# Kernel optimization log

Hardware: AMD Instinct MI355X
Metric: run time of the kernel (lower is better)

Reference implementation:

```python
import math
import jax, jax.numpy as jnp
import numpy as np

B, N, D = 32, 1025, 768
K, CD, TD = 64, 128, 256  # num_clusters, cluster_dim, token_dim
REG = 0.1
NUM_ITERS = 5


def setup_inputs() -> dict:
    key = jax.random.key(0)
    ks = jax.random.split(key, 8)
    x = jax.random.normal(ks[0], (B, N, D), dtype=jnp.float32)
    # Linear params (torch nn.Linear: y = x @ W.T + b; we store W already transposed as [in, out])
    Wf = jax.random.normal(ks[1], (D, CD), dtype=jnp.float32) / math.sqrt(D)
    bf = jnp.zeros((CD,), dtype=jnp.float32)
    Ws = jax.random.normal(ks[2], (D, K), dtype=jnp.float32) / math.sqrt(D)
    bs = jnp.zeros((K,), dtype=jnp.float32)
    Wt = jax.random.normal(ks[3], (D, TD), dtype=jnp.float32) / math.sqrt(D)
    bt = jnp.zeros((TD,), dtype=jnp.float32)
    anchors = jax.random.normal(ks[4], (K, CD), dtype=jnp.float32) * 0.1
    dust_bin = jnp.float32(1.0)
    sharpness = jnp.float32(5.0)
    return {"x": x, "Wf": Wf, "bf": bf, "Ws": Ws, "bs": bs, "Wt": Wt, "bt": bt,
            "anchors": anchors, "dust_bin": dust_bin, "sharpness": sharpness}


def _log_otp_solver(log_a, log_b, M, num_iters, reg):
    M = M / reg
    u = jnp.zeros_like(log_a)  # [B, K+1]
    v = jnp.zeros_like(log_b)  # [B, N-1]
    for _ in range(num_iters):
        u = log_a - jax.nn.logsumexp(M + v[:, None, :], axis=2)
        v = log_b - jax.nn.logsumexp(M + u[:, :, None], axis=1)
    return M + u[:, :, None] + v[:, None, :]


def reference(x, Wf, bf, Ws, bs, Wt, bt, anchors, dust_bin, sharpness):
    b, n, d = x.shape
    t_global = x[:, 0]            # [B, D]
    fi = x[:, 1:]                 # [B, N-1, D]
    f = fi @ Wf + bf              # [B, N-1, CD]
    s = jnp.swapaxes(fi @ Ws + bs, 1, 2)  # [B, K, N-1]
    t = t_global @ Wt + bt        # [B, TD]
    s = s * sharpness
    dust = jnp.broadcast_to(dust_bin, (b, 1, n - 1))
    s_aug = jnp.concatenate([s, dust], axis=1)  # [B, K+1, N-1]
    log_a = jnp.full((b, K + 1), -math.log(K + 1), dtype=x.dtype)
    log_b = jnp.full((b, n - 1), -math.log(n - 1), dtype=x.dtype)
    log_P = _log_otp_solver(log_a, log_b, s_aug, NUM_ITERS, REG)
    p = jnp.exp(log_P)[:, :-1, :]  # [B, K, N-1]
    # v_agg = sum_n p[b,k,n] * (2*f[b,n,:] - anchors[k,:])  (algebraic rewrite of the broadcast sum)
    v_agg = 2.0 * jnp.einsum('bkn,bnc->bkc', p, f) - p.sum(axis=2)[:, :, None] * anchors[None]
    v_local = v_agg.reshape(b, -1)            # [B, K*CD]
    f_out = jnp.concatenate([t, v_local], axis=-1)
    norm = jnp.maximum(jnp.linalg.norm(f_out, axis=-1, keepdims=True), 1e-12)
    return f_out / norm
```

## Files before the change

### kernel.cpp

```cpp
#include <hip/hip_runtime.h>
#include <math.h>


#define BATCH 32
#define NTOK  1025
#define DIM   768
#define KDIM  64
#define CDIM  128
#define TDIM  256
#define NM1   1024
#define ROWLEN 8448
#define NITER 5
#define INV_REG 10.0f
#define NSPLIT 16
#define LOG_A (-4.17438727f)
#define LOG_B (-6.93147181f)

typedef __attribute__((ext_vector_type(8))) short short8;
typedef __attribute__((ext_vector_type(4))) float floatx4;

typedef __attribute__((address_space(3))) unsigned int lds_uint;
typedef const __attribute__((address_space(1))) unsigned int glb_uint;

__device__ __forceinline__ void gload_lds16(const void* g, void* l) {
    __builtin_amdgcn_global_load_lds((glb_uint*)g, (lds_uint*)l, 16, 0, 0);
}

__device__ __forceinline__ unsigned short bf16_rne(float f) {
    unsigned u = __builtin_bit_cast(unsigned, f);
    unsigned r = u + 0x7FFFu + ((u >> 16) & 1u);
    return (unsigned short)(r >> 16);
}

__device__ __forceinline__ short8 cvt8(float4 a, float4 b) {
    short8 r;
    r[0] = (short)bf16_rne(a.x); r[1] = (short)bf16_rne(a.y);
    r[2] = (short)bf16_rne(a.z); r[3] = (short)bf16_rne(a.w);
    r[4] = (short)bf16_rne(b.x); r[5] = (short)bf16_rne(b.y);
    r[6] = (short)bf16_rne(b.z); r[7] = (short)bf16_rne(b.w);
    return r;
}

__global__ __launch_bounds__(256) void pack_w(
    const float* __restrict__ Wf, const float* __restrict__ Ws,
    const float* __restrict__ bf, const float* __restrict__ bs,
    short* __restrict__ W_pack, float* __restrict__ bias_all)
{
    int idx = blockIdx.x * 256 + threadIdx.x;
    if (idx < 24 * 12 * 512) {
        int g    = idx / 6144;
        int rem  = idx - g * 6144;
        int nf   = rem >> 9;
        int rem2 = rem & 511;
        int lane = rem2 >> 3;
        int j    = rem2 & 7;
        int k = g * 32 + (lane >> 4) * 8 + j;
        int c = nf * 16 + (lane & 15);
        float v = (c < CDIM) ? Wf[(size_t)k * CDIM + c] : Ws[(size_t)k * KDIM + (c - CDIM)];
        W_pack[idx] = (short)bf16_rne(v);
    }
    if (idx < 192) bias_all[idx] = (idx < CDIM) ? bf[idx] : bs[idx - CDIM];
}

__global__ __launch_bounds__(256, 2) void gemm_fs(
    const float* __restrict__ x, const short* __restrict__ W_pack,
    const float* __restrict__ bias_all, const float* __restrict__ sharp_p,
    float* __restrict__ fmat, float* __restrict__ Mmat)
{
    __shared__ __align__(16) short Bs[12288];
    __shared__ __align__(16) short As[4096];
    const int tid  = threadIdx.x;
    const int wave = tid >> 6, lane = tid & 63;
    const int quad = lane >> 4, lrow = lane & 15;
    const int R = blockIdx.x * 64 + wave * 16;

    const int arow = blockIdx.x * 64 + (tid >> 2);
    const float* asrc = x + ((size_t)(arow >> 10) * NTOK + 1 + (arow & 1023)) * DIM + (tid & 3) * 16;
    const int r    = (tid >> 2) & 15;
    const int seg  = tid & 3;
    const int kk_w = seg >> 1;
    const int q0   = (seg & 1) * 2;
    short* adst0 = &As[(((tid >> 6) * 2 + kk_w) * 64 + q0 * 16 + r) * 8];
    short* adst1 = &As[(((tid >> 6) * 2 + kk_w) * 64 + (q0 + 1) * 16 + r) * 8];

    floatx4 acc[12];
#pragma unroll
    for (int nf = 0; nf < 12; ++nf) acc[nf] = (floatx4){0.f, 0.f, 0.f, 0.f};

    for (int ko = 0; ko < 12; ++ko) {
        __syncthreads();
        const short* bsrc = W_pack + ko * 12288 + tid * 8;
#pragma unroll
        for (int i = 0; i < 6; ++i)
            gload_lds16(bsrc + i * 2048, &Bs[i * 2048 + tid * 8]);
        {
            const float* ap = asrc + ko * 64;
            float4 g0 = *(const float4*)(ap);
            float4 g1 = *(const float4*)(ap + 4);
            float4 g2 = *(const float4*)(ap + 8);
            float4 g3 = *(const float4*)(ap + 12);
            *(short8*)adst0 = cvt8(g0, g1);
            *(short8*)adst1 = cvt8(g2, g3);
        }
        __syncthreads();
#pragma unroll
        for (int kk = 0; kk < 2; ++kk) {
            short8 af = *(const short8*)&As[((wave * 2 + kk) * 64 + lane) * 8];
#pragma unroll
            for (int nf = 0; nf < 12; ++nf) {
                short8 bf8 = *(const short8*)&Bs[((kk * 12 + nf) * 64 + lane) * 8];
                acc[nf] = __builtin_amdgcn_mfma_f32_16x16x32_bf16(af, bf8, acc[nf], 0, 0, 0);
            }
        }
    }

    const float sc = sharp_p[0] * INV_REG;
    const int bb = R >> 10;
    const int n0 = (R & 1023) + quad * 4;
#pragma unroll
    for (int nf = 0; nf < 12; ++nf) {
        const int c = nf * 16 + lrow;
        const float bias = bias_all[c];
        if (nf < 8) {
            float* fp = fmat + ((size_t)R + quad * 4) * CDIM + c;
#pragma unroll
            for (int j = 0; j < 4; ++j)
                fp[(size_t)j * CDIM] = acc[nf][j] + bias;
        } else {
            const int k = c - CDIM;
            float4 w = make_float4((acc[nf][0] + bias) * sc, (acc[nf][1] + bias) * sc,
                                   (acc[nf][2] + bias) * sc, (acc[nf][3] + bias) * sc);
            *(float4*)(Mmat + ((size_t)bb * KDIM + k) * NM1 + n0) = w;
        }
    }
}

__global__ __launch_bounds__(256) void gemm_t_split(
    const float* __restrict__ x, const float* __restrict__ Wt,
    float* __restrict__ tpart)
{
    __shared__ float xr[256];
    const int b = blockIdx.x, dy = blockIdx.y, c = threadIdx.x;
    xr[c] = x[(size_t)b * NTOK * DIM + (size_t)dy * 256 + c];
    __syncthreads();
    float acc = 0.f;
    const float* wp = Wt + (size_t)dy * 256 * TDIM + c;
#pragma unroll 8
    for (int d = 0; d < 256; ++d) acc = fmaf(xr[d], wp[(size_t)d * TDIM], acc);
    tpart[((size_t)dy * BATCH + b) * TDIM + c] = acc;
}

__global__ __launch_bounds__(256) void sink_u(
    const float* __restrict__ Mmat, const float* __restrict__ v_in,
    const float* __restrict__ dust_p, float* __restrict__ u_out)
{
    const int wv   = (blockIdx.x << 2) + (threadIdx.x >> 6);
    const int lane = threadIdx.x & 63;
    const int b = wv / 65, k = wv - b * 65;
    const float dustM = dust_p[0] * INV_REG;

    const float4* vp = (const float4*)(v_in + (size_t)b * NM1);
    float xs[16];
    if (k < 64) {
        const float4* Mp = (const float4*)(Mmat + ((size_t)b * KDIM + k) * NM1);
#pragma unroll
        for (int i = 0; i < 4; ++i) {
            float4 mv = Mp[i * 64 + lane];
            float4 vv = vp[i * 64 + lane];
            xs[i * 4 + 0] = mv.x + vv.x;
            xs[i * 4 + 1] = mv.y + vv.y;
            xs[i * 4 + 2] = mv.z + vv.z;
            xs[i * 4 + 3] = mv.w + vv.w;
        }
    } else {
#pragma unroll
        for (int i = 0; i < 4; ++i) {
            float4 vv = vp[i * 64 + lane];
            xs[i * 4 + 0] = dustM + vv.x;
            xs[i * 4 + 1] = dustM + vv.y;
            xs[i * 4 + 2] = dustM + vv.z;
            xs[i * 4 + 3] = dustM + vv.w;
        }
    }
    float m = xs[0];
#pragma unroll
    for (int i = 1; i < 16; ++i) m = fmaxf(m, xs[i]);
#pragma unroll
    for (int off = 1; off < 64; off <<= 1) m = fmaxf(m, __shfl_xor(m, off));
    float S = 0.f;
#pragma unroll
    for (int i = 0; i < 16; ++i) S += __expf(xs[i] - m);
#pragma unroll
    for (int off = 1; off < 64; off <<= 1) S += __shfl_xor(S, off);
    if (lane == 0) u_out[wv] = LOG_A - (m + __logf(S));
}

__global__ __launch_bounds__(256) void sink_v(
    const float* __restrict__ Mmat, const float* __restrict__ u_in,
    const float* __restrict__ dust_p, float* __restrict__ v_out)
{
    __shared__ float us[65];
    const int b = blockIdx.x, tid = threadIdx.x;
    const int n = blockIdx.y * 256 + tid;
    if (tid < 65) us[tid] = u_in[b * 65 + tid];
    __syncthreads();
    const float* Mb = Mmat + (size_t)b * KDIM * NM1 + n;
    float xs[64];
#pragma unroll
    for (int k = 0; k < 64; ++k) xs[k] = Mb[(size_t)k * NM1] + us[k];
    const float xd = dust_p[0] * INV_REG + us[64];
    float m = xd;
#pragma unroll
    for (int k = 0; k < 64; ++k) m = fmaxf(m, xs[k]);
    float S = __expf(xd - m);
#pragma unroll
    for (int k = 0; k < 64; ++k) S += __expf(xs[k] - m);
    v_out[(size_t)b * NM1 + n] = LOG_B - (m + __logf(S));
}

__global__ __launch_bounds__(128) void aggregate(
    const float* __restrict__ Mmat, const float* __restrict__ fmat,
    const float* __restrict__ u_in, const float* __restrict__ v_in,
    float* __restrict__ vpart, float* __restrict__ rspart)
{
    __shared__ float fs[32 * 128];
    __shared__ float ps[32 * 68];
    __shared__ float us[KDIM];
    __shared__ float vsh[64];
    const int b = blockIdx.x, ns = blockIdx.y;
    const int tid = threadIdx.x;
    const int tx = tid & 7;
    const int ty = tid >> 3;
    const int n0 = ns * 64;

    if (tid < 64) us[tid] = u_in[b * 65 + tid];
    else          vsh[tid - 64] = v_in[(size_t)b * NM1 + n0 + (tid - 64)];

    const float* Mb = Mmat + (size_t)b * KDIM * NM1;
    const float* fb = fmat + ((size_t)b * NM1 + n0) * CDIM;

    float acc[8][8];
#pragma unroll
    for (int i = 0; i < 8; ++i)
#pragma unroll
        for (int j = 0; j < 8; ++j) acc[i][j] = 0.f;
    float rsacc = 0.f;

    const int p_nn = tid & 31;
    const int p_kb = tid >> 5;

    for (int ch = 0; ch < 2; ++ch) {
        __syncthreads();
        {
            const float* fsrc = fb + (size_t)(ch * 32) * CDIM;
#pragma unroll
            for (int q = 0; q < 8; ++q) {
                int idx = q * 128 + tid;
                int nn = idx >> 5, c4 = (idx & 31) * 4;
                *(float4*)&fs[nn * 128 + c4] = *(const float4*)(fsrc + (size_t)nn * CDIM + c4);
            }
        }
        {
            int nglob = n0 + ch * 32 + p_nn;
            float vv = vsh[ch * 32 + p_nn];
#pragma unroll
            for (int q = 0; q < 16; ++q) {
                int k = q * 4 + p_kb;
                ps[p_nn * 68 + k] = __expf(Mb[(size_t)k * NM1 + nglob] + us[k] + vv);
            }
        }
        __syncthreads();
        if (tid < 64) {
#pragma unroll
            for (int nn = 0; nn < 32; ++nn) rsacc += ps[nn * 68 + tid];
        }
#pragma unroll
        for (int nn = 0; nn < 32; ++nn) {
            float4 p0 = *(const float4*)&ps[nn * 68 + tx * 8];
            float4 p1 = *(const float4*)&ps[nn * 68 + tx * 8 + 4];
            float4 f0 = *(const float4*)&fs[nn * 128 + ty * 8];
            float4 f1 = *(const float4*)&fs[nn * 128 + ty * 8 + 4];
            float pv[8] = {p0.x, p0.y, p0.z, p0.w, p1.x, p1.y, p1.z, p1.w};
            float fv[8] = {f0.x, f0.y, f0.z, f0.w, f1.x, f1.y, f1.z, f1.w};
#pragma unroll
            for (int i = 0; i < 8; ++i)
#pragma unroll
                for (int j = 0; j < 8; ++j)
                    acc[i][j] = fmaf(pv[i], fv[j], acc[i][j]);
        }
    }

    float* vp = vpart + (size_t)(ns * BATCH + b) * (KDIM * CDIM);
#pragma unroll
    for (int i = 0; i < 8; ++i) {
        int k = tx * 8 + i;
        float4 w0 = make_float4(acc[i][0], acc[i][1], acc[i][2], acc[i][3]);
        float4 w1 = make_float4(acc[i][4], acc[i][5], acc[i][6], acc[i][7]);
        float* wp = vp + (size_t)k * CDIM + ty * 8;
        *(float4*)(wp)     = w0;
        *(float4*)(wp + 4) = w1;
    }
    if (tid < 64) rspart[(ns * BATCH + b) * KDIM + tid] = rsacc;
}

__global__ __launch_bounds__(256) void reduce_vagg(
    const float* __restrict__ vpart, const float* __restrict__ rspart,
    const float* __restrict__ anchors, float* __restrict__ vagg,
    float* __restrict__ sq)
{
    __shared__ float rst[8];
    __shared__ float red[4];
    const int b = blockIdx.x, segi = blockIdx.y, tid = threadIdx.x;
    const int lane = tid & 63, wave = tid >> 6;
    if (tid < 8) {
        float s = 0.f;
#pragma unroll
        for (int ns = 0; ns < NSPLIT; ++ns)
            s += rspart[(ns * BATCH + b) * KDIM + segi * 8 + tid];
        rst[tid] = s;
    }
    __syncthreads();
    const int i4 = segi * 256 + tid;
    float4 s = make_float4(0.f, 0.f, 0.f, 0.f);
#pragma unroll
    for (int ns = 0; ns < NSPLIT; ++ns) {
        const float4 v = *(const float4*)&vpart[(size_t)(ns * BATCH + b) * (KDIM * CDIM) + (size_t)i4 * 4];
        s.x += v.x; s.y += v.y; s.z += v.z; s.w += v.w;
    }
    float rs = rst[tid >> 5];
    const float4 an = *(const float4*)&anchors[(size_t)i4 * 4];
    float4 v;
    v.x = 2.f * s.x - rs * an.x;
    v.y = 2.f * s.y - rs * an.y;
    v.z = 2.f * s.z - rs * an.z;
    v.w = 2.f * s.w - rs * an.w;
    *(float4*)&vagg[(size_t)b * (KDIM * CDIM) + (size_t)i4 * 4] = v;
    float ss = v.x * v.x + v.y * v.y + v.z * v.z + v.w * v.w;
#pragma unroll
    for (int off = 32; off > 0; off >>= 1) ss += __shfl_down(ss, off);
    if (lane == 0) red[wave] = ss;
    __syncthreads();
    if (tid == 0) sq[b * 8 + segi] = red[0] + red[1] + red[2] + red[3];
}

__global__ __launch_bounds__(256) void finalize2(
    const float* __restrict__ tpart, const float* __restrict__ bt,
    const float* __restrict__ sq, const float* __restrict__ vagg,
    float* __restrict__ out)
{
    __shared__ float red[4];
    __shared__ float sc_sh;
    const int b = blockIdx.x, tid = threadIdx.x;
    const int lane = tid & 63, wave = tid >> 6;

    float t = bt[tid];
#pragma unroll
    for (int s = 0; s < 3; ++s) t += tpart[((size_t)s * BATCH + b) * TDIM + tid];
    float ss = t * t;
#pragma unroll
    for (int off = 32; off > 0; off >>= 1) ss += __shfl_down(ss, off);
    if (lane == 0) red[wave] = ss;
    __syncthreads();
    if (tid == 0) {
        float tot = red[0] + red[1] + red[2] + red[3];
#pragma unroll
        for (int i = 0; i < 8; ++i) tot += sq[b * 8 + i];
        sc_sh = 1.f / fmaxf(sqrtf(tot), 1e-12f);
    }
    __syncthreads();
    const float scale = sc_sh;
    float* orow = out + (size_t)b * ROWLEN;
    orow[tid] = t * scale;
    const float* va = vagg + (size_t)b * (KDIM * CDIM);
#pragma unroll
    for (int q = 0; q < 8; ++q) {
        int i4 = q * 256 + tid;
        float4 v = *(const float4*)&va[(size_t)i4 * 4];
        v.x *= scale; v.y *= scale; v.z *= scale; v.w *= scale;
        *(float4*)&orow[TDIM + (size_t)i4 * 4] = v;
    }
}

extern "C" void kernel_launch(void* const* d_in, const int* in_sizes, int n_in,
                              void* d_out, int out_size, void* d_ws, size_t ws_size,
                              hipStream_t stream)
{
    const float* x       = (const float*)d_in[0];
    const float* Wf      = (const float*)d_in[1];
    const float* bf      = (const float*)d_in[2];
    const float* Ws      = (const float*)d_in[3];
    const float* bs      = (const float*)d_in[4];
    const float* Wt      = (const float*)d_in[5];
    const float* bt      = (const float*)d_in[6];
    const float* anchors = (const float*)d_in[7];
    const float* dust    = (const float*)d_in[8];
    const float* sharp   = (const float*)d_in[9];
    float* out = (float*)d_out;

    char* base = (char*)d_ws;
    short* W_pack   = (short*)base;
    float* bias_all = (float*)(base + 294912);
    float* Mmat     = bias_all + 192;
    float* fmat     = Mmat + (size_t)BATCH * KDIM * NM1;
    float* u_buf    = fmat + (size_t)BATCH * NM1 * CDIM;
    float* v_buf    = u_buf + BATCH * 65;
    float* vpart    = v_buf + BATCH * NM1;
    float* rspart   = vpart + (size_t)NSPLIT * BATCH * KDIM * CDIM;
    float* tpart    = rspart + NSPLIT * BATCH * KDIM;
    float* sq       = tpart + 3 * BATCH * TDIM;
    float* vagg     = Mmat;

    hipLaunchKernelGGL(pack_w, dim3(576), dim3(256), 0, stream,
                       Wf, Ws, bf, bs, W_pack, bias_all);
    hipLaunchKernelGGL(gemm_fs, dim3(512), dim3(256), 0, stream,
                       x, W_pack, bias_all, sharp, fmat, Mmat);
    hipLaunchKernelGGL(gemm_t_split, dim3(BATCH, 3), dim3(256), 0, stream,
                       x, Wt, tpart);

    hipMemsetAsync(v_buf, 0, (size_t)BATCH * NM1 * sizeof(float), stream);
    for (int it = 0; it < NITER; ++it) {
        hipLaunchKernelGGL(sink_u, dim3(520), dim3(256), 0, stream,
                           Mmat, v_buf, dust, u_buf);
        hipLaunchKernelGGL(sink_v, dim3(BATCH, 4), dim3(256), 0, stream,
                           Mmat, u_buf, dust, v_buf);
    }

    hipLaunchKernelGGL(aggregate, dim3(BATCH, NSPLIT), dim3(128), 0, stream,
                       Mmat, fmat, u_buf, v_buf, vpart, rspart);
    hipLaunchKernelGGL(reduce_vagg, dim3(BATCH, 8), dim3(256), 0, stream,
                       vpart, rspart, anchors, vagg, sq);
    hipLaunchKernelGGL(finalize2, dim3(BATCH), dim3(256), 0, stream,
                       tpart, bt, sq, vagg, out);
}
```

Before: 257.9 us.

## Prefetch GEMM A tiles, specialize first Sinkhorn step, and widen sink_v/aggregate grids

Software-prefetches the next A tile in gemm_fs into registers so global loads overlap the MFMA loop. The first sink_u is specialized to skip reading v, which removes the memset. sink_v runs twice as many 128-thread blocks. aggregate moves to NSPLIT=32 with 256 threads, each handling 32 tokens in one pass, giving more parallelism at the cost of twice the partial sums for reduce_vagg to read.

```diff
diff --git a/kernel.cpp b/kernel.cpp
--- a/kernel.cpp
+++ b/kernel.cpp
@@ -12,7 +12,7 @@
 #define ROWLEN 8448
 #define NITER 5
 #define INV_REG 10.0f
-#define NSPLIT 16
+#define NSPLIT 32
 #define LOG_A (-4.17438727f)
 #define LOG_B (-6.93147181f)
 
@@ -87,20 +87,25 @@
 #pragma unroll
     for (int nf = 0; nf < 12; ++nf) acc[nf] = (floatx4){0.f, 0.f, 0.f, 0.f};
 
+    float4 g0 = *(const float4*)(asrc);
+    float4 g1 = *(const float4*)(asrc + 4);
+    float4 g2 = *(const float4*)(asrc + 8);
+    float4 g3 = *(const float4*)(asrc + 12);
+
     for (int ko = 0; ko < 12; ++ko) {
         __syncthreads();
         const short* bsrc = W_pack + ko * 12288 + tid * 8;
 #pragma unroll
         for (int i = 0; i < 6; ++i)
             gload_lds16(bsrc + i * 2048, &Bs[i * 2048 + tid * 8]);
-        {
-            const float* ap = asrc + ko * 64;
-            float4 g0 = *(const float4*)(ap);
-            float4 g1 = *(const float4*)(ap + 4);
-            float4 g2 = *(const float4*)(ap + 8);
-            float4 g3 = *(const float4*)(ap + 12);
-            *(short8*)adst0 = cvt8(g0, g1);
-            *(short8*)adst1 = cvt8(g2, g3);
+        *(short8*)adst0 = cvt8(g0, g1);
+        *(short8*)adst1 = cvt8(g2, g3);
+        if (ko < 11) {
+            const float* ap = asrc + (ko + 1) * 64;
+            g0 = *(const float4*)(ap);
+            g1 = *(const float4*)(ap + 4);
+            g2 = *(const float4*)(ap + 8);
+            g3 = *(const float4*)(ap + 12);
         }
         __syncthreads();
 #pragma unroll
@@ -150,6 +155,7 @@
     tpart[((size_t)dy * BATCH + b) * TDIM + c] = acc;
 }
 
+template<bool FIRST>
 __global__ __launch_bounds__(256) void sink_u(
     const float* __restrict__ Mmat, const float* __restrict__ v_in,
     const float* __restrict__ dust_p, float* __restrict__ u_out)
@@ -166,7 +172,7 @@
 #pragma unroll
         for (int i = 0; i < 4; ++i) {
             float4 mv = Mp[i * 64 + lane];
-            float4 vv = vp[i * 64 + lane];
+            float4 vv = FIRST ? make_float4(0.f, 0.f, 0.f, 0.f) : vp[i * 64 + lane];
             xs[i * 4 + 0] = mv.x + vv.x;
             xs[i * 4 + 1] = mv.y + vv.y;
             xs[i * 4 + 2] = mv.z + vv.z;
@@ -175,7 +181,7 @@
     } else {
 #pragma unroll
         for (int i = 0; i < 4; ++i) {
-            float4 vv = vp[i * 64 + lane];
+            float4 vv = FIRST ? make_float4(0.f, 0.f, 0.f, 0.f) : vp[i * 64 + lane];
             xs[i * 4 + 0] = dustM + vv.x;
             xs[i * 4 + 1] = dustM + vv.y;
             xs[i * 4 + 2] = dustM + vv.z;
@@ -195,13 +201,13 @@
     if (lane == 0) u_out[wv] = LOG_A - (m + __logf(S));
 }
 
-__global__ __launch_bounds__(256) void sink_v(
+__global__ __launch_bounds__(128) void sink_v(
     const float* __restrict__ Mmat, const float* __restrict__ u_in,
     const float* __restrict__ dust_p, float* __restrict__ v_out)
 {
     __shared__ float us[65];
     const int b = blockIdx.x, tid = threadIdx.x;
-    const int n = blockIdx.y * 256 + tid;
+    const int n = blockIdx.y * 128 + tid;
     if (tid < 65) us[tid] = u_in[b * 65 + tid];
     __syncthreads();
     const float* Mb = Mmat + (size_t)b * KDIM * NM1 + n;
@@ -218,7 +224,7 @@
     v_out[(size_t)b * NM1 + n] = LOG_B - (m + __logf(S));
 }
 
-__global__ __launch_bounds__(128) void aggregate(
+__global__ __launch_bounds__(256) void aggregate(
     const float* __restrict__ Mmat, const float* __restrict__ fmat,
     const float* __restrict__ u_in, const float* __restrict__ v_in,
     float* __restrict__ vpart, float* __restrict__ rspart)
@@ -226,79 +232,66 @@
     __shared__ float fs[32 * 128];
     __shared__ float ps[32 * 68];
     __shared__ float us[KDIM];
-    __shared__ float vsh[64];
+    __shared__ float vsh[32];
     const int b = blockIdx.x, ns = blockIdx.y;
     const int tid = threadIdx.x;
     const int tx = tid & 7;
     const int ty = tid >> 3;
-    const int n0 = ns * 64;
+    const int n0 = ns * 32;
 
     if (tid < 64) us[tid] = u_in[b * 65 + tid];
-    else          vsh[tid - 64] = v_in[(size_t)b * NM1 + n0 + (tid - 64)];
-
-    const float* Mb = Mmat + (size_t)b * KDIM * NM1;
+    else if (tid < 96) vsh[tid - 64] = v_in[(size_t)b * NM1 + n0 + (tid - 64)];
+    __syncthreads();
+
     const float* fb = fmat + ((size_t)b * NM1 + n0) * CDIM;
-
-    float acc[8][8];
+#pragma unroll
+    for (int q = 0; q < 4; ++q) {
+        int idx = q * 256 + tid;
+        int nn = idx >> 5, c4 = (idx & 31) * 4;
+        *(float4*)&fs[nn * 128 + c4] = *(const float4*)(fb + (size_t)nn * CDIM + c4);
+    }
+    {
+        const int p_nn = tid & 31, p_kb = tid >> 5;
+        const float* Mb = Mmat + (size_t)b * KDIM * NM1 + n0 + p_nn;
+        const float vv = vsh[p_nn];
+#pragma unroll
+        for (int q = 0; q < 8; ++q) {
+            int k = q * 8 + p_kb;
+            ps[p_nn * 68 + k] = __expf(Mb[(size_t)k * NM1] + us[k] + vv);
+        }
+    }
+    __syncthreads();
+
+    float rsacc = 0.f;
+    if (tid < 64) {
+#pragma unroll
+        for (int nn = 0; nn < 32; ++nn) rsacc += ps[nn * 68 + tid];
+    }
+    float acc[8][4];
 #pragma unroll
     for (int i = 0; i < 8; ++i)
 #pragma unroll
-        for (int j = 0; j < 8; ++j) acc[i][j] = 0.f;
-    float rsacc = 0.f;
-
-    const int p_nn = tid & 31;
-    const int p_kb = tid >> 5;
-
-    for (int ch = 0; ch < 2; ++ch) {
-        __syncthreads();
-        {
-            const float* fsrc = fb + (size_t)(ch * 32) * CDIM;
-#pragma unroll
-            for (int q = 0; q < 8; ++q) {
-                int idx = q * 128 + tid;
-                int nn = idx >> 5, c4 = (idx & 31) * 4;
-                *(float4*)&fs[nn * 128 + c4] = *(const float4*)(fsrc + (size_t)nn * CDIM + c4);
-            }
-        }
-        {
-            int nglob = n0 + ch * 32 + p_nn;
-            float vv = vsh[ch * 32 + p_nn];
-#pragma unroll
-            for (int q = 0; q < 16; ++q) {
-                int k = q * 4 + p_kb;
-                ps[p_nn * 68 + k] = __expf(Mb[(size_t)k * NM1 + nglob] + us[k] + vv);
-            }
-        }
-        __syncthreads();
-        if (tid < 64) {
-#pragma unroll
-            for (int nn = 0; nn < 32; ++nn) rsacc += ps[nn * 68 + tid];
-        }
-#pragma unroll
-        for (int nn = 0; nn < 32; ++nn) {
-            float4 p0 = *(const float4*)&ps[nn * 68 + tx * 8];
-            float4 p1 = *(const float4*)&ps[nn * 68 + tx * 8 + 4];
-            float4 f0 = *(const float4*)&fs[nn * 128 + ty * 8];
-            float4 f1 = *(const float4*)&fs[nn * 128 + ty * 8 + 4];
-            float pv[8] = {p0.x, p0.y, p0.z, p0.w, p1.x, p1.y, p1.z, p1.w};
-            float fv[8] = {f0.x, f0.y, f0.z, f0.w, f1.x, f1.y, f1.z, f1.w};
-#pragma unroll
-            for (int i = 0; i < 8; ++i)
-#pragma unroll
-                for (int j = 0; j < 8; ++j)
-                    acc[i][j] = fmaf(pv[i], fv[j], acc[i][j]);
-        }
+        for (int j = 0; j < 4; ++j) acc[i][j] = 0.f;
+#pragma unroll
+    for (int nn = 0; nn < 32; ++nn) {
+        float4 p0 = *(const float4*)&ps[nn * 68 + tx * 8];
+        float4 p1 = *(const float4*)&ps[nn * 68 + tx * 8 + 4];
+        float4 f0 = *(const float4*)&fs[nn * 128 + ty * 4];
+        float pv[8] = {p0.x, p0.y, p0.z, p0.w, p1.x, p1.y, p1.z, p1.w};
+        float fv[4] = {f0.x, f0.y, f0.z, f0.w};
+#pragma unroll
+        for (int i = 0; i < 8; ++i)
+#pragma unroll
+            for (int j = 0; j < 4; ++j)
+                acc[i][j] = fmaf(pv[i], fv[j], acc[i][j]);
     }
 
     float* vp = vpart + (size_t)(ns * BATCH + b) * (KDIM * CDIM);
 #pragma unroll
     for (int i = 0; i < 8; ++i) {
         int k = tx * 8 + i;
-        float4 w0 = make_float4(acc[i][0], acc[i][1], acc[i][2], acc[i][3]);
-        float4 w1 = make_float4(acc[i][4], acc[i][5], acc[i][6], acc[i][7]);
-        float* wp = vp + (size_t)k * CDIM + ty * 8;
-        *(float4*)(wp)     = w0;
-        *(float4*)(wp + 4) = w1;
+        *(float4*)(vp + (size_t)k * CDIM + ty * 4) =
+            make_float4(acc[i][0], acc[i][1], acc[i][2], acc[i][3]);
     }
     if (tid < 64) rspart[(ns * BATCH + b) * KDIM + tid] = rsacc;
 }
@@ -417,15 +410,18 @@
     hipLaunchKernelGGL(gemm_t_split, dim3(BATCH, 3), dim3(256), 0, stream,
                        x, Wt, tpart);
 
-    hipMemsetAsync(v_buf, 0, (size_t)BATCH * NM1 * sizeof(float), stream);
-    for (int it = 0; it < NITER; ++it) {
-        hipLaunchKernelGGL(sink_u, dim3(520), dim3(256), 0, stream,
+    hipLaunchKernelGGL(HIP_KERNEL_NAME(sink_u<true>), dim3(520), dim3(256), 0, stream,
+                       Mmat, v_buf, dust, u_buf);
+    hipLaunchKernelGGL(sink_v, dim3(BATCH, 8), dim3(128), 0, stream,
+                       Mmat, u_buf, dust, v_buf);
+    for (int it = 1; it < NITER; ++it) {
+        hipLaunchKernelGGL(HIP_KERNEL_NAME(sink_u<false>), dim3(520), dim3(256), 0, stream,
                            Mmat, v_buf, dust, u_buf);
-        hipLaunchKernelGGL(sink_v, dim3(BATCH, 4), dim3(256), 0, stream,
+        hipLaunchKernelGGL(sink_v, dim3(BATCH, 8), dim3(128), 0, stream,
                            Mmat, u_buf, dust, v_buf);
     }
 
-    hipLaunchKernelGGL(aggregate, dim3(BATCH, NSPLIT), dim3(128), 0, stream,
+    hipLaunchKernelGGL(aggregate, dim3(BATCH, NSPLIT), dim3(256), 0, stream,
                        Mmat, fmat, u_buf, v_buf, vpart, rspart);
     hipLaunchKernelGGL(reduce_vagg, dim3(BATCH, 8), dim3(256), 0, stream,
                        vpart, rspart, anchors, vagg, sq);
```

After: 248.1 us. 3.8% less time.
